# Kernel tuning notes

Hardware: AMD Instinct MI355X
Metric: run time of the kernel (lower is better)

The kernel has to match this reference:

```python
import jax, jax.numpy as jnp
import numpy as np

PATCH = 8

def setup_inputs() -> dict:
    key = jax.random.key(0)
    k0, k1, k2, k3 = jax.random.split(key, 4)
    dim = 128
    hidden = int(dim * 3)
    B, H, W = 4, 256, 256
    x = jax.random.normal(k0, (B, dim, H, W), jnp.float32)
    # project_in: Conv2d(dim, 2*hidden, k=1, bias=False) -> weight [2h, dim]
    w_in = jax.random.normal(k1, (2 * hidden, dim), jnp.float32) * 0.02
    # dwconv: Conv2d(2h, 2h, k=3, groups=2h) -> depthwise kernel [2h, 1, 3, 3]
    w_dw = jax.random.normal(k2, (2 * hidden, 1, 3, 3), jnp.float32) * 0.1
    # spectral filter, initialized to ones as in the module
    fft_filter = jnp.ones((dim, 1, 1, PATCH, PATCH // 2 + 1), jnp.float32)
    # project_out: Conv2d(hidden, dim, k=1) -> weight [dim, hidden]
    w_out = jax.random.normal(k3, (dim, hidden), jnp.float32) * 0.02
    return {"x": x, "w_in": w_in, "w_dw": w_dw, "fft_filter": fft_filter, "w_out": w_out}


def reference(x, w_in, w_dw, fft_filter, w_out):
    P = PATCH
    # 1x1 project_in: [B, dim, H, W] -> [B, 2h, H, W]
    h = jnp.einsum('oi,bihw->bohw', w_in, x)
    # 3x3 depthwise conv, SAME padding
    h = jax.lax.conv_general_dilated(
        h, w_dw, window_strides=(1, 1), padding='SAME',
        dimension_numbers=('NCHW', 'OIHW', 'NCHW'),
        feature_group_count=h.shape[1])
    x1, x2 = jnp.split(h, 2, axis=1)
    g = jax.nn.gelu(x1, approximate=False) * x2  # torch F.gelu is exact erf
    # 1x1 project_out: [B, hidden, H, W] -> [B, dim, H, W]
    y = jnp.einsum('oi,bihw->bohw', w_out, g)
    b, c, H, W = y.shape
    hn = (P - H % P) % P
    wn = (P - W % P) % P
    if hn or wn:
        y = jnp.pad(y, ((0, 0), (0, 0), (0, hn), (0, wn)), mode='reflect')
    Hp, Wp = y.shape[2], y.shape[3]
    # b c (h p1) (w p2) -> b c h w p1 p2
    yp = y.reshape(b, c, Hp // P, P, Wp // P, P).transpose(0, 1, 2, 4, 3, 5)
    yf = jnp.fft.rfft2(yp)                 # [b, c, h, w, P, P//2+1] complex
    yf = yf * fft_filter                   # broadcast over (c,1,1,P,P//2+1)
    yp = jnp.fft.irfft2(yf, s=(P, P))
    y = yp.transpose(0, 1, 2, 4, 3, 5).reshape(b, c, Hp, Wp)
    return y[:, :, :H, :W]
```

## Files before the change

kernel.cpp:

```cpp
#include <hip/hip_runtime.h>

typedef _Float16 f16;
typedef _Float16 f16x2 __attribute__((ext_vector_type(2)));
typedef _Float16 f16x4 __attribute__((ext_vector_type(4)));
typedef _Float16 f16x8 __attribute__((ext_vector_type(8)));
typedef __fp16  fp16x2 __attribute__((ext_vector_type(2)));
typedef float f32x4 __attribute__((ext_vector_type(4)));

#define DIM  128
#define HID  384
#define HID2 768
#define NPX  65536
#define NB   4

static __device__ __forceinline__ f16x2 bc2(unsigned u) {
    union { unsigned u; f16x2 h; } x; x.u = u; return x.h;
}

__global__ __launch_bounds__(256) void k_prep_w(
    const float* __restrict__ w_in, const float* __restrict__ w_out,
    const float* __restrict__ w_dw,
    f16* __restrict__ wibf, f16* __restrict__ wob, f16* __restrict__ wpkT)
{
    int i = blockIdx.x * 256 + threadIdx.x;
    if (i < HID2 * DIM) {
        int j = i & 7, l = (i >> 3) & 63, ni = (i >> 9) & 3;
        int wn = (i >> 11) & 1, kk = (i >> 12) & 3, cN = i >> 14;
        int lr = l & 15, lh = l >> 4;
        int n = wn*64 + ni*16 + lr;
        int row = (n < 64) ? cN*64 + n : 384 + cN*64 + (n - 64);
        wibf[i] = (f16)w_in[row*128 + kk*32 + lh*8 + j];
    }
    if (i < DIM * HID)  wob[i] = (f16)w_out[i];
    if (i < 9 * HID2) {
        int k = i / HID2, ch = i - k * HID2;
        wpkT[i] = (f16)w_dw[ch * 9 + k];
    }
}

__global__ void k_ktab(const float* __restrict__ filt, float* __restrict__ ktab,
                       int* __restrict__ isdelta)
{
    int c = blockIdx.x, t = threadIdx.x;
    int a = t >> 3, bb = t & 7;
    const float ct[8] = {1.f, 0.70710678118654752f, 0.f, -0.70710678118654752f,
                        -1.f, -0.70710678118654752f, 0.f, 0.70710678118654752f};
    float s = 0.f;
    for (int u = 0; u < 8; ++u)
        for (int v = 0; v < 8; ++v) {
            float Guv = (v <= 4) ? filt[c*40 + u*5 + v]
                                 : filt[c*40 + ((8-u)&7)*5 + (8-v)];
            s += Guv * ct[(u*a + v*bb) & 7];
        }
    s *= (1.f/64.f);
    ktab[c*64 + t] = s;
    float want = (t == 0) ? 1.f : 0.f;
    unsigned long long m = __ballot(fabsf(s - want) < 1e-5f);
    if (t == 0) isdelta[c] = (m == 0xFFFFFFFFFFFFFFFFULL) ? 1 : 0;
}

__global__ __launch_bounds__(256) void k_transpose(
    const float* __restrict__ x, f16* __restrict__ xt)
{
    __shared__ float tile[64][65];
    const int b = blockIdx.z;
    const float* xb = x + (size_t)b * DIM * NPX;
    f16* xtb = xt + (size_t)b * NPX * DIM;
    const int c0 = blockIdx.y * 64, p0 = blockIdx.x * 64;
    for (int i = threadIdx.x; i < 4096; i += 256) {
        int cl = i >> 6, pl = i & 63;
        tile[pl][cl] = xb[(size_t)(c0+cl)*NPX + p0 + pl];
    }
    __syncthreads();
    for (int i = threadIdx.x; i < 2048; i += 256) {
        int pl = i >> 5, c2 = (i & 31) * 2;
        f16x2 v = { (f16)tile[pl][c2], (f16)tile[pl][c2+1] };
        *(f16x2*)&xtb[(size_t)(p0+pl)*DIM + c0 + c2] = v;
    }
}

__global__ __launch_bounds__(256, 2) void k_fused(
    const f16* __restrict__ xt, const f16* __restrict__ wibf,
    const f16* __restrict__ wpkT, f16* __restrict__ g)
{
    __shared__ f16 As[128*128];
    __shared__ f16 h1s[64*132];
    __shared__ f16 h2s[64*132];

    const int t  = threadIdx.x;
    const int tx = (blockIdx.x & 31) * 8;
    const int ty = (blockIdx.x >> 5) * 8;
    const f16* xtb = xt + (size_t)blockIdx.y * NPX * DIM;
    f16* gb = g + (size_t)blockIdx.y * NPX * HID;

#pragma unroll
    for (int j = 0; j < 8; ++j) {
        int i = t + j*256;
        int m = i >> 4, c8 = i & 15;
        int hr = (m * 683) >> 13;
        int hc = m - hr*12;
        int gy = ty - 1 + hr, gx = tx - 1 + hc;
        f16x8 v = {0,0,0,0,0,0,0,0};
        if (hr < 10 && hc < 10 && (unsigned)gy < 256u && (unsigned)gx < 256u)
            v = *(const f16x8*)&xtb[(size_t)(gy*256 + gx)*DIM + c8*8];
        *(f16x8*)&As[(m*128 + c8*8) ^ ((m & 7) << 3)] = v;
    }
    __syncthreads();

    const int l = t & 63, w = t >> 6, lr = l & 15, lh = l >> 4;
    const int wm = w >> 1, wn = w & 1;
    const int sch = t & 63;
    const int spy = (t >> 6) * 2;

    unsigned Ap[4][6], Up[4][4];
    f16x2 w2[9];
    f16x2 acc2a[2][4], acc2b[2][4];

#define STEN_LOAD(HB, CHOFF)                                                     \
    { _Pragma("unroll")                                                          \
      for (int r = 0; r < 4; ++r) {                                              \
        const f16* rp = &HB[sch*132 + (spy + r)*12];                             \
        uint2 q0 = *(const uint2*)(rp);                                          \
        uint2 q1 = *(const uint2*)(rp + 4);                                      \
        uint2 q2 = *(const uint2*)(rp + 8);                                      \
        Ap[r][0]=q0.x; Ap[r][1]=q0.y; Ap[r][2]=q1.x;                             \
        Ap[r][3]=q1.y; Ap[r][4]=q2.x; Ap[r][5]=q2.y;                             \
        Up[r][0]=__builtin_amdgcn_alignbit(Ap[r][1],Ap[r][0],16);                \
        Up[r][1]=__builtin_amdgcn_alignbit(Ap[r][2],Ap[r][1],16);                \
        Up[r][2]=__builtin_amdgcn_alignbit(Ap[r][3],Ap[r][2],16);                \
        Up[r][3]=__builtin_amdgcn_alignbit(Ap[r][4],Ap[r][3],16);                \
      }                                                                          \
      _Pragma("unroll")                                                          \
      for (int k = 0; k < 9; ++k) {                                              \
        f16 wv = wpkT[k*HID2 + (CHOFF) + cs*64 + sch];                           \
        w2[k] = (f16x2){wv, wv};                                                 \
      } }

#define STEN_FMA(ACC2)                                                           \
    { _Pragma("unroll")                                                          \
      for (int rr = 0; rr < 2; ++rr) {                                           \
        _Pragma("unroll")                                                        \
        for (int j = 0; j < 4; ++j) ACC2[rr][j] = (f16x2){0,0};                  \
        _Pragma("unroll")                                                        \
        for (int dy = 0; dy < 3; ++dy) {                                         \
          int r = rr + dy;                                                       \
          _Pragma("unroll")                                                      \
          for (int j = 0; j < 4; ++j) {                                          \
            ACC2[rr][j] = __builtin_elementwise_fma(bc2(Ap[r][j]),   w2[dy*3+0], ACC2[rr][j]); \
            ACC2[rr][j] = __builtin_elementwise_fma(bc2(Up[r][j]),   w2[dy*3+1], ACC2[rr][j]); \
            ACC2[rr][j] = __builtin_elementwise_fma(bc2(Ap[r][j+1]), w2[dy*3+2], ACC2[rr][j]); \
          } } } }

#define GATE_STORE()                                                             \
    { _Pragma("unroll")                                                          \
      for (int rr = 0; rr < 2; ++rr) {                                           \
        const int oy = spy + rr;                                                 \
        _Pragma("unroll")                                                        \
        for (int j = 0; j < 4; ++j) {                                            \
          _Pragma("unroll")                                                      \
          for (int hf = 0; hf < 2; ++hf) {                                       \
            float av_ = (float)acc2a[rr][j][hf];                                 \
            float bv_ = (float)acc2b[rr][j][hf];                                 \
            float z  = av_ * 0.70710678118654752f;                               \
            float z2 = z * z;                                                    \
            float er = z * (1.1283791671f + z2*(-0.3761263890f                   \
                         + z2*0.1128379167f));                                   \
            er = fminf(1.0f, fmaxf(-1.0f, er));                                  \
            float ge = 0.5f * av_ * (1.0f + er);                                 \
            gb[((size_t)((ty + oy)*256 + tx + j*2 + hf))*HID + cs*64 + sch]      \
                = (f16)(ge * bv_);                                               \
          } } } }

    for (int cN = 0; cN < 6; ++cN) {
        const bool doS = (cN > 0);
        const int  cs  = cN - 1;

        f32x4 acc[4][4];
#pragma unroll
        for (int mi = 0; mi < 4; ++mi)
#pragma unroll
            for (int ni = 0; ni < 4; ++ni) acc[mi][ni] = (f32x4){0.f,0.f,0.f,0.f};

#pragma unroll
        for (int kk = 0; kk < 4; ++kk) {
            f16x8 avf[4], bvf[4];
#pragma unroll
            for (int mi = 0; mi < 4; ++mi) {
                int r = wm*64 + mi*16 + lr;
                avf[mi] = *(const f16x8*)&As[(r*128 + kk*32 + lh*8) ^ ((r & 7) << 3)];
            }
#pragma unroll
            for (int ni = 0; ni < 4; ++ni)
                bvf[ni] = *(const f16x8*)
                    &wibf[((((cN*4 + kk)*2 + wn)*4 + ni)*64 + l) * 8];
            __builtin_amdgcn_s_setprio(1);
#pragma unroll
            for (int mi = 0; mi < 4; ++mi)
#pragma unroll
                for (int ni = 0; ni < 4; ++ni)
                    acc[mi][ni] = __builtin_amdgcn_mfma_f32_16x16x32_f16(
                        avf[mi], bvf[ni], acc[mi][ni], 0, 0, 0);
            __builtin_amdgcn_s_setprio(0);

            if (doS) {
                if (kk == 0) { STEN_LOAD(h1s, 0) }
                if (kk == 1) { STEN_FMA(acc2a) }
                if (kk == 2) { STEN_LOAD(h2s, HID) }
                if (kk == 3) { STEN_FMA(acc2b) }
            }
        }
        if (doS) { GATE_STORE() }

        __syncthreads();
        {
            f16* hb = (wn == 0) ? h1s : h2s;
#pragma unroll
            for (int mi = 0; mi < 4; ++mi)
#pragma unroll
                for (int ni = 0; ni < 4; ++ni) {
                    int ch = ni*16 + lr;
                    int m  = wm*64 + mi*16 + lh*4;
                    union { struct { fp16x2 a, b; } p; f16x4 v; } u;
                    u.p.a = __builtin_amdgcn_cvt_pkrtz(acc[mi][ni][0], acc[mi][ni][1]);
                    u.p.b = __builtin_amdgcn_cvt_pkrtz(acc[mi][ni][2], acc[mi][ni][3]);
                    *(f16x4*)&hb[ch*132 + m] = u.v;
                }
        }
        __syncthreads();
    }

    {
        const int cs = 5;
        STEN_LOAD(h1s, 0)
        STEN_FMA(acc2a)
        STEN_LOAD(h2s, HID)
        STEN_FMA(acc2b)
        GATE_STORE()
    }
#undef STEN_LOAD
#undef STEN_FMA
#undef GATE_STORE
}

__global__ __launch_bounds__(256) void k_gemm2sp(
    const f16* __restrict__ g, const f16* __restrict__ wob,
    const float* __restrict__ ktab, const int* __restrict__ isdelta,
    float* __restrict__ out)
{
    __shared__ __attribute__((aligned(16))) char smem[65536];
    f16*   Al = (f16*)smem;
    f16*   Bl = (f16*)(smem + 16384);
    float* yl = (float*)smem;

    const int px0 = blockIdx.x * 16;
    const int py0 = blockIdx.y * 8;
    const int b   = blockIdx.z;
    const f16* gb = g + (size_t)b * NPX * HID;
    float* outb = out + (size_t)b * DIM * NPX;
    const int t = threadIdx.x;
    const int l = t & 63, w = t >> 6, lr = l & 15, lh = l >> 4;
    const int wm = w >> 1, wn = w & 1;

    f32x4 acc[4][4];
#pragma unroll
    for (int mi = 0; mi < 4; ++mi)
#pragma unroll
        for (int ni = 0; ni < 4; ++ni) acc[mi][ni] = (f32x4){0.f, 0.f, 0.f, 0.f};

    for (int k0 = 0; k0 < HID; k0 += 64) {
#pragma unroll
        for (int i = t; i < 1024; i += 256) {
            int row = i >> 3, c8 = i & 7;
            int so = (row*64 + c8*8) ^ ((row & 7) << 3);
            int pxl = (py0 + (row >> 4))*256 + px0 + (row & 15);
            *(f16x8*)&Al[so] = *(const f16x8*)&gb [(size_t)pxl*HID + k0 + c8*8];
            *(f16x8*)&Bl[so] = *(const f16x8*)&wob[(size_t)row*HID + k0 + c8*8];
        }
        __syncthreads();
#pragma unroll
        for (int kk = 0; kk < 2; ++kk) {
            f16x8 av[4], bv[4];
#pragma unroll
            for (int mi = 0; mi < 4; ++mi) {
                int r = wm*64 + mi*16 + lr;
                av[mi] = *(const f16x8*)&Al[(r*64 + kk*32 + lh*8) ^ ((r & 7) << 3)];
            }
#pragma unroll
            for (int ni = 0; ni < 4; ++ni) {
                int r = wn*64 + ni*16 + lr;
                bv[ni] = *(const f16x8*)&Bl[(r*64 + kk*32 + lh*8) ^ ((r & 7) << 3)];
            }
#pragma unroll
            for (int mi = 0; mi < 4; ++mi)
#pragma unroll
                for (int ni = 0; ni < 4; ++ni)
                    acc[mi][ni] = __builtin_amdgcn_mfma_f32_16x16x32_f16(
                        av[mi], bv[ni], acc[mi][ni], 0, 0, 0);
        }
        __syncthreads();
    }

#pragma unroll
    for (int mi = 0; mi < 4; ++mi)
#pragma unroll
        for (int ni = 0; ni < 4; ++ni) {
            int o = wn*64 + ni*16 + lr;
#pragma unroll
            for (int r = 0; r < 4; ++r) {
                int m = wm*64 + mi*16 + lh*4 + r;
                int c16 = m & 15, pr = m >> 4;
                int p = c16 >> 3, ppx = pr*8 + (c16 & 7);
                yl[(size_t)(p*64 + ppx)*128 + o] = acc[mi][ni][r];
            }
        }
    __syncthreads();

    const int c = t & 127, half = t >> 7;
    for (int p = 0; p < 2; ++p) {
        const float* ylp = &yl[(size_t)p*64*128];
        const int pxb = px0 + p*8;
        if (isdelta[c]) {
#pragma unroll
            for (int r = 0; r < 4; ++r) {
                int pl = half*4 + r;
                float o0[8];
#pragma unroll
                for (int xx = 0; xx < 8; ++xx) o0[xx] = ylp[(pl*8 + xx)*128 + c];
                size_t ob = (size_t)c*NPX + (size_t)(py0 + pl)*256 + pxb;
                *(float4*)&outb[ob]     = make_float4(o0[0], o0[1], o0[2], o0[3]);
                *(float4*)&outb[ob + 4] = make_float4(o0[4], o0[5], o0[6], o0[7]);
            }
        } else {
            const float* kc = &ktab[c*64];
            for (int r = 0; r < 4; ++r) {
                int pyl = half*4 + r;
                float o0[8];
                for (int xx = 0; xx < 8; ++xx) {
                    float s = 0.f;
                    for (int a = 0; a < 8; ++a)
                        for (int bb = 0; bb < 8; ++bb)
                            s += kc[a*8 + bb] *
                                 ylp[(((pyl - a) & 7)*8 + ((xx - bb) & 7))*128 + c];
                    o0[xx] = s;
                }
                size_t ob = (size_t)c*NPX + (size_t)(py0 + pyl)*256 + pxb;
                *(float4*)&outb[ob]     = make_float4(o0[0], o0[1], o0[2], o0[3]);
                *(float4*)&outb[ob + 4] = make_float4(o0[4], o0[5], o0[6], o0[7]);
            }
        }
    }
}

__global__ void k_diag(float* out, float v) { out[0] = v; }

extern "C" void kernel_launch(void* const* d_in, const int* in_sizes, int n_in,
                              void* d_out, int out_size, void* d_ws, size_t ws_size,
                              hipStream_t stream)
{
    const float* x     = (const float*)d_in[0];
    const float* w_in  = (const float*)d_in[1];
    const float* w_dw  = (const float*)d_in[2];
    const float* filt  = (const float*)d_in[3];
    const float* w_out = (const float*)d_in[4];
    float* out = (float*)d_out;
    char* ws = (char*)d_ws;

    const size_t OFF_WIB = 0;
    const size_t OFF_WOB = 196608;
    const size_t OFF_KT  = OFF_WOB + 98304;
    const size_t OFF_ISD = OFF_KT + 32768;
    const size_t OFF_WPK = OFF_ISD + 512;
    const size_t WEND    = 524288;

    const size_t SZ_XT = (size_t)NB * NPX * DIM * 2;
    const size_t SZ_G  = (size_t)NB * NPX * HID * 2;
    const size_t NEED  = WEND + SZ_XT + SZ_G;
    if (ws_size < NEED) {
        k_diag<<<1, 1, 0, stream>>>(out, (float)((double)ws_size / 1048576.0));
        return;
    }

    f16*   wibf = (f16*)(ws + OFF_WIB);
    f16*   wob  = (f16*)(ws + OFF_WOB);
    float* kt   = (float*)(ws + OFF_KT);
    int*   isd  = (int*)(ws + OFF_ISD);
    f16*   wpk  = (f16*)(ws + OFF_WPK);
    f16*   xt   = (f16*)(ws + WEND);
    f16*   g    = (f16*)(ws + WEND + SZ_XT);

    k_prep_w<<<dim3(384), dim3(256), 0, stream>>>(w_in, w_out, w_dw, wibf, wob, wpk);
    k_ktab<<<dim3(128), dim3(64), 0, stream>>>(filt, kt, isd);
    k_transpose<<<dim3(1024, 2, NB), dim3(256), 0, stream>>>(x, xt);
    k_fused<<<dim3(1024, NB), dim3(256), 0, stream>>>(xt, wibf, wpk, g);
    k_gemm2sp<<<dim3(16, 32, NB), dim3(256), 0, stream>>>(g, wob, kt, isd, out);
}
```

Measured before the change: 390.8 us.

## Fuse project_out GEMM and spectral filter into fused conv kernel

Folds the second 1x1 projection and the per-patch spectral convolution into k_fused. Each gated chunk is staged in shared memory and fed to MFMA against a pre-swizzled w_out, so the large f16 intermediate g no longer makes a global round trip and the separate k_gemm2sp launch goes away. The trade-off is more shared memory per block, which is reused through a union, plus extra MFMA work and syncs inside the already heavy fused kernel. Occupancy may drop.

```diff
diff --git a/kernel.cpp b/kernel.cpp
--- a/kernel.cpp
+++ b/kernel.cpp
@@ -20,7 +20,7 @@
 __global__ __launch_bounds__(256) void k_prep_w(
     const float* __restrict__ w_in, const float* __restrict__ w_out,
     const float* __restrict__ w_dw,
-    f16* __restrict__ wibf, f16* __restrict__ wob, f16* __restrict__ wpkT)
+    f16* __restrict__ wibf, f16* __restrict__ wobf, f16* __restrict__ wpkT)
 {
     int i = blockIdx.x * 256 + threadIdx.x;
     if (i < HID2 * DIM) {
@@ -31,7 +31,14 @@
         int row = (n < 64) ? cN*64 + n : 384 + cN*64 + (n - 64);
         wibf[i] = (f16)w_in[row*128 + kk*32 + lh*8 + j];
     }
-    if (i < DIM * HID)  wob[i] = (f16)w_out[i];
+    if (i < DIM * HID) {
+        int j = i & 7, l = (i >> 3) & 63, ni = (i >> 9) & 3;
+        int wn = (i >> 11) & 1, kk2 = (i >> 12) & 1, cs = i >> 13;
+        int lr = l & 15, lh = l >> 4;
+        int ch_out = wn*64 + ni*16 + lr;
+        int ch_in  = cs*64 + kk2*32 + lh*8 + j;
+        wobf[i] = (f16)w_out[ch_out*HID + ch_in];
+    }
     if (i < 9 * HID2) {
         int k = i / HID2, ch = i - k * HID2;
         wpkT[i] = (f16)w_dw[ch * 9 + k];
@@ -81,17 +88,22 @@
 
 __global__ __launch_bounds__(256, 2) void k_fused(
     const f16* __restrict__ xt, const f16* __restrict__ wibf,
-    const f16* __restrict__ wpkT, f16* __restrict__ g)
-{
-    __shared__ f16 As[128*128];
+    const f16* __restrict__ wobf, const f16* __restrict__ wpkT,
+    const float* __restrict__ ktab, const int* __restrict__ isdelta,
+    float* __restrict__ out)
+{
+    __shared__ __attribute__((aligned(16))) char uni[33792];
     __shared__ f16 h1s[64*132];
     __shared__ f16 h2s[64*132];
+    __shared__ f16 gAs[64*64];
+    f16*   As = (f16*)uni;
+    float* yl = (float*)uni;
 
     const int t  = threadIdx.x;
     const int tx = (blockIdx.x & 31) * 8;
     const int ty = (blockIdx.x >> 5) * 8;
     const f16* xtb = xt + (size_t)blockIdx.y * NPX * DIM;
-    f16* gb = g + (size_t)blockIdx.y * NPX * HID;
+    float* outb = out + (size_t)blockIdx.y * DIM * NPX;
 
 #pragma unroll
     for (int j = 0; j < 8; ++j) {
@@ -115,6 +127,11 @@
     unsigned Ap[4][6], Up[4][4];
     f16x2 w2[9];
     f16x2 acc2a[2][4], acc2b[2][4];
+    f32x4 accY[2][4];
+#pragma unroll
+    for (int mi = 0; mi < 2; ++mi)
+#pragma unroll
+        for (int ni = 0; ni < 4; ++ni) accY[mi][ni] = (f32x4){0.f,0.f,0.f,0.f};
 
 #define STEN_LOAD(HB, CHOFF)                                                     \
     { _Pragma("unroll")                                                          \
@@ -151,7 +168,7 @@
             ACC2[rr][j] = __builtin_elementwise_fma(bc2(Ap[r][j+1]), w2[dy*3+2], ACC2[rr][j]); \
           } } } }
 
-#define GATE_STORE()                                                             \
+#define GATE_GA()                                                                \
     { _Pragma("unroll")                                                          \
       for (int rr = 0; rr < 2; ++rr) {                                           \
         const int oy = spy + rr;                                                 \
@@ -167,9 +184,29 @@
                          + z2*0.1128379167f));                                   \
             er = fminf(1.0f, fmaxf(-1.0f, er));                                  \
             float ge = 0.5f * av_ * (1.0f + er);                                 \
-            gb[((size_t)((ty + oy)*256 + tx + j*2 + hf))*HID + cs*64 + sch]      \
-                = (f16)(ge * bv_);                                               \
+            int jx = j*2 + hf;                                                   \
+            gAs[(oy*8 + jx)*64 + (sch ^ (jx << 3))] = (f16)(ge * bv_);           \
           } } } }
+
+#define GEMM2(CS)                                                                \
+    { _Pragma("unroll")                                                          \
+      for (int kk2 = 0; kk2 < 2; ++kk2) {                                        \
+        f16x8 a2[2], b2[4];                                                      \
+        _Pragma("unroll")                                                        \
+        for (int mi = 0; mi < 2; ++mi) {                                         \
+          int row = wm*32 + mi*16 + lr;                                          \
+          a2[mi] = *(const f16x8*)&gAs[row*64 + ((kk2*32 + lh*8) ^ ((row&7)<<3))]; \
+        }                                                                        \
+        _Pragma("unroll")                                                        \
+        for (int ni = 0; ni < 4; ++ni)                                           \
+          b2[ni] = *(const f16x8*)&wobf[(((((CS)*2 + kk2)*2 + wn)*4 + ni)*64 + l)*8]; \
+        _Pragma("unroll")                                                        \
+        for (int mi = 0; mi < 2; ++mi)                                           \
+          _Pragma("unroll")                                                      \
+          for (int ni = 0; ni < 4; ++ni)                                         \
+            accY[mi][ni] = __builtin_amdgcn_mfma_f32_16x16x32_f16(               \
+                a2[mi], b2[ni], accY[mi][ni], 0, 0, 0);                          \
+      } }
 
     for (int cN = 0; cN < 6; ++cN) {
         const bool doS = (cN > 0);
@@ -209,9 +246,11 @@
                 if (kk == 3) { STEN_FMA(acc2b) }
             }
         }
-        if (doS) { GATE_STORE() }
+        if (doS) { GATE_GA() }
 
         __syncthreads();
+        if (doS) { GEMM2(cs) }
+
         {
             f16* hb = (wn == 0) ? h1s : h2s;
 #pragma unroll
@@ -235,120 +274,58 @@
         STEN_FMA(acc2a)
         STEN_LOAD(h2s, HID)
         STEN_FMA(acc2b)
-        GATE_STORE()
+        GATE_GA()
+        __syncthreads();
+        GEMM2(5)
+    }
+
+#pragma unroll
+    for (int mi = 0; mi < 2; ++mi)
+#pragma unroll
+        for (int ni = 0; ni < 4; ++ni) {
+            int ch = wn*64 + ni*16 + lr;
+#pragma unroll
+            for (int r = 0; r < 4; ++r) {
+                int px = wm*32 + mi*16 + lh*4 + r;
+                yl[px*132 + ch] = accY[mi][ni][r];
+            }
+        }
+    __syncthreads();
+
+    const int c = t & 127, half = t >> 7;
+    if (isdelta[c]) {
+#pragma unroll
+        for (int r = 0; r < 4; ++r) {
+            int pl = half*4 + r;
+            float o0[8];
+#pragma unroll
+            for (int xx = 0; xx < 8; ++xx) o0[xx] = yl[(pl*8 + xx)*132 + c];
+            size_t ob = (size_t)c*NPX + (size_t)(ty + pl)*256 + tx;
+            *(float4*)&outb[ob]     = make_float4(o0[0], o0[1], o0[2], o0[3]);
+            *(float4*)&outb[ob + 4] = make_float4(o0[4], o0[5], o0[6], o0[7]);
+        }
+    } else {
+        const float* kc = &ktab[c*64];
+        for (int r = 0; r < 4; ++r) {
+            int pyl = half*4 + r;
+            float o0[8];
+            for (int xx = 0; xx < 8; ++xx) {
+                float s = 0.f;
+                for (int a = 0; a < 8; ++a)
+                    for (int bb = 0; bb < 8; ++bb)
+                        s += kc[a*8 + bb] *
+                             yl[(((pyl - a) & 7)*8 + ((xx - bb) & 7))*132 + c];
+                o0[xx] = s;
+            }
+            size_t ob = (size_t)c*NPX + (size_t)(ty + pyl)*256 + tx;
+            *(float4*)&outb[ob]     = make_float4(o0[0], o0[1], o0[2], o0[3]);
+            *(float4*)&outb[ob + 4] = make_float4(o0[4], o0[5], o0[6], o0[7]);
+        }
     }
 #undef STEN_LOAD
 #undef STEN_FMA
-#undef GATE_STORE
-}
-
-__global__ __launch_bounds__(256) void k_gemm2sp(
-    const f16* __restrict__ g, const f16* __restrict__ wob,
-    const float* __restrict__ ktab, const int* __restrict__ isdelta,
-    float* __restrict__ out)
-{
-    __shared__ __attribute__((aligned(16))) char smem[65536];
-    f16*   Al = (f16*)smem;
-    f16*   Bl = (f16*)(smem + 16384);
-    float* yl = (float*)smem;
-
-    const int px0 = blockIdx.x * 16;
-    const int py0 = blockIdx.y * 8;
-    const int b   = blockIdx.z;
-    const f16* gb = g + (size_t)b * NPX * HID;
-    float* outb = out + (size_t)b * DIM * NPX;
-    const int t = threadIdx.x;
-    const int l = t & 63, w = t >> 6, lr = l & 15, lh = l >> 4;
-    const int wm = w >> 1, wn = w & 1;
-
-    f32x4 acc[4][4];
-#pragma unroll
-    for (int mi = 0; mi < 4; ++mi)
-#pragma unroll
-        for (int ni = 0; ni < 4; ++ni) acc[mi][ni] = (f32x4){0.f, 0.f, 0.f, 0.f};
-
-    for (int k0 = 0; k0 < HID; k0 += 64) {
-#pragma unroll
-        for (int i = t; i < 1024; i += 256) {
-            int row = i >> 3, c8 = i & 7;
-            int so = (row*64 + c8*8) ^ ((row & 7) << 3);
-            int pxl = (py0 + (row >> 4))*256 + px0 + (row & 15);
-            *(f16x8*)&Al[so] = *(const f16x8*)&gb [(size_t)pxl*HID + k0 + c8*8];
-            *(f16x8*)&Bl[so] = *(const f16x8*)&wob[(size_t)row*HID + k0 + c8*8];
-        }
-        __syncthreads();
-#pragma unroll
-        for (int kk = 0; kk < 2; ++kk) {
-            f16x8 av[4], bv[4];
-#pragma unroll
-            for (int mi = 0; mi < 4; ++mi) {
-                int r = wm*64 + mi*16 + lr;
-                av[mi] = *(const f16x8*)&Al[(r*64 + kk*32 + lh*8) ^ ((r & 7) << 3)];
-            }
-#pragma unroll
-            for (int ni = 0; ni < 4; ++ni) {
-                int r = wn*64 + ni*16 + lr;
-                bv[ni] = *(const f16x8*)&Bl[(r*64 + kk*32 + lh*8) ^ ((r & 7) << 3)];
-            }
-#pragma unroll
-            for (int mi = 0; mi < 4; ++mi)
-#pragma unroll
-                for (int ni = 0; ni < 4; ++ni)
-                    acc[mi][ni] = __builtin_amdgcn_mfma_f32_16x16x32_f16(
-                        av[mi], bv[ni], acc[mi][ni], 0, 0, 0);
-        }
-        __syncthreads();
-    }
-
-#pragma unroll
-    for (int mi = 0; mi < 4; ++mi)
-#pragma unroll
-        for (int ni = 0; ni < 4; ++ni) {
-            int o = wn*64 + ni*16 + lr;
-#pragma unroll
-            for (int r = 0; r < 4; ++r) {
-                int m = wm*64 + mi*16 + lh*4 + r;
-                int c16 = m & 15, pr = m >> 4;
-                int p = c16 >> 3, ppx = pr*8 + (c16 & 7);
-                yl[(size_t)(p*64 + ppx)*128 + o] = acc[mi][ni][r];
-            }
-        }
-    __syncthreads();
-
-    const int c = t & 127, half = t >> 7;
-    for (int p = 0; p < 2; ++p) {
-        const float* ylp = &yl[(size_t)p*64*128];
-        const int pxb = px0 + p*8;
-        if (isdelta[c]) {
-#pragma unroll
-            for (int r = 0; r < 4; ++r) {
-                int pl = half*4 + r;
-                float o0[8];
-#pragma unroll
-                for (int xx = 0; xx < 8; ++xx) o0[xx] = ylp[(pl*8 + xx)*128 + c];
-                size_t ob = (size_t)c*NPX + (size_t)(py0 + pl)*256 + pxb;
-                *(float4*)&outb[ob]     = make_float4(o0[0], o0[1], o0[2], o0[3]);
-                *(float4*)&outb[ob + 4] = make_float4(o0[4], o0[5], o0[6], o0[7]);
-            }
-        } else {
-            const float* kc = &ktab[c*64];
-            for (int r = 0; r < 4; ++r) {
-                int pyl = half*4 + r;
-                float o0[8];
-                for (int xx = 0; xx < 8; ++xx) {
-                    float s = 0.f;
-                    for (int a = 0; a < 8; ++a)
-                        for (int bb = 0; bb < 8; ++bb)
-                            s += kc[a*8 + bb] *
-                                 ylp[(((pyl - a) & 7)*8 + ((xx - bb) & 7))*128 + c];
-                    o0[xx] = s;
-                }
-                size_t ob = (size_t)c*NPX + (size_t)(py0 + pyl)*256 + pxb;
-                *(float4*)&outb[ob]     = make_float4(o0[0], o0[1], o0[2], o0[3]);
-                *(float4*)&outb[ob + 4] = make_float4(o0[4], o0[5], o0[6], o0[7]);
-            }
-        }
-    }
+#undef GATE_GA
+#undef GEMM2
 }
 
 __global__ void k_diag(float* out, float v) { out[0] = v; }
@@ -373,24 +350,21 @@
     const size_t WEND    = 524288;
 
     const size_t SZ_XT = (size_t)NB * NPX * DIM * 2;
-    const size_t SZ_G  = (size_t)NB * NPX * HID * 2;
-    const size_t NEED  = WEND + SZ_XT + SZ_G;
+    const size_t NEED  = WEND + SZ_XT;
     if (ws_size < NEED) {
         k_diag<<<1, 1, 0, stream>>>(out, (float)((double)ws_size / 1048576.0));
         return;
     }
 
     f16*   wibf = (f16*)(ws + OFF_WIB);
-    f16*   wob  = (f16*)(ws + OFF_WOB);
+    f16*   wobf = (f16*)(ws + OFF_WOB);
     float* kt   = (float*)(ws + OFF_KT);
     int*   isd  = (int*)(ws + OFF_ISD);
     f16*   wpk  = (f16*)(ws + OFF_WPK);
     f16*   xt   = (f16*)(ws + WEND);
-    f16*   g    = (f16*)(ws + WEND + SZ_XT);
-
-    k_prep_w<<<dim3(384), dim3(256), 0, stream>>>(w_in, w_out, w_dw, wibf, wob, wpk);
+
+    k_prep_w<<<dim3(384), dim3(256), 0, stream>>>(w_in, w_out, w_dw, wibf, wobf, wpk);
     k_ktab<<<dim3(128), dim3(64), 0, stream>>>(filt, kt, isd);
     k_transpose<<<dim3(1024, 2, NB), dim3(256), 0, stream>>>(x, xt);
-    k_fused<<<dim3(1024, NB), dim3(256), 0, stream>>>(xt, wibf, wpk, g);
-    k_gemm2sp<<<dim3(16, 32, NB), dim3(256), 0, stream>>>(g, wob, kt, isd, out);
-}
+    k_fused<<<dim3(1024, NB), dim3(256), 0, stream>>>(xt, wibf, wobf, wpk, kt, isd, out);
+}
```

Measured after the change: 359.8 us. 8.0% less time.
